# Kernel optimization log

Measured on AMD Instinct MI355X. Metric: run time of the kernel, lower is better.

## Reference

```python
import jax, jax.numpy as jnp
import numpy as np

H = 128
R = 14
B = 2048
TYPES = ['operator', 'table', 'column', 'predicate', 'operation', 'literal', 'numeral']
SIZES = {'operator': 100000, 'table': 20000, 'column': 120000, 'predicate': 60000,
         'operation': 100000, 'literal': 50000, 'numeral': 50000}
FEAT = {'operator': 4, 'table': 2, 'column': 10, 'predicate': 4, 'operation': 8,
        'literal': 1, 'numeral': 1}
# (name, src_type, dst_type, num_edges), order matches edge_type_mapping in the torch module
EDGES = [('ei_scannedby', 'table', 'operator', 100000),
         ('ei_pred_filters', 'predicate', 'operator', 100000),
         ('ei_outputby', 'column', 'operator', 100000),
         ('ei_col_connects', 'column', 'operation', 100000),
         ('ei_calledby', 'operator', 'operator', 100000),
         ('ei_op_filters', 'operation', 'operator', 100000),
         ('ei_op_connects', 'operation', 'predicate', 100000),
         ('ei_lit_connects', 'literal', 'operation', 100000),
         ('ei_num_connects', 'numeral', 'operation', 100000),
         ('ei_lit_self', 'literal', 'literal', 50000),
         ('ei_num_self', 'numeral', 'numeral', 50000),
         ('ei_tab_self', 'table', 'table', 20000),
         ('ei_col_self', 'column', 'column', 120000),
         ('ei_pred_self', 'predicate', 'predicate', 60000)]
OFFS = {}
_o = 0
for _t in TYPES:
    OFFS[_t] = _o
    _o += SIZES[_t]
N_TOTAL = _o


def setup_inputs():
    key = jax.random.key(0)
    ks = iter(jax.random.split(key, 64))
    inp = {}
    for t in TYPES:
        inp['x_' + t] = jax.random.normal(next(ks), (SIZES[t], FEAT[t]), jnp.float32)
    for name, s, d, E in EDGES:
        src = jax.random.randint(next(ks), (E,), 0, SIZES[s], jnp.int32)
        dst = jax.random.randint(next(ks), (E,), 0, SIZES[d], jnp.int32)
        inp[name] = jnp.stack([src, dst])
    inp['batch_operator'] = jnp.sort(
        jax.random.randint(next(ks), (SIZES['operator'],), 0, B, jnp.int32))

    def lin_w(k, din, dout):
        s = 1.0 / float(np.sqrt(din))
        return jax.random.uniform(k, (din, dout), jnp.float32, -s, s)

    for t in TYPES:
        inp['W_' + t] = lin_w(next(ks), FEAT[t], H)
        inp['b_' + t] = jnp.zeros((H,), jnp.float32)
    for c in ('c1', 'c2'):
        inp[c + '_root'] = lin_w(next(ks), H, H)
        inp[c + '_rel'] = jax.random.normal(next(ks), (R, H, H), jnp.float32) / float(np.sqrt(H))
        inp[c + '_bias'] = jnp.zeros((H,), jnp.float32)
    inp['n1_g'] = jnp.ones((H,), jnp.float32); inp['n1_b'] = jnp.zeros((H,), jnp.float32)
    inp['n2_g'] = jnp.ones((H,), jnp.float32); inp['n2_b'] = jnp.zeros((H,), jnp.float32)
    inp['W_lin'] = lin_w(next(ks), H, 1)
    inp['b_lin'] = jnp.zeros((1,), jnp.float32)
    return inp


def layer_norm(x, g, b, eps=1e-5):
    mu = jnp.mean(x, axis=-1, keepdims=True)
    var = jnp.var(x, axis=-1, keepdims=True)
    return (x - mu) * jax.lax.rsqrt(var + eps) * g + b


def rgcn(x, rel_edges, w_root, w_rel, bias):
    # PyG RGCNConv: root transform + per-relation gather -> GEMM -> scatter-mean into dst
    out = x @ w_root
    for r, (src, dst) in enumerate(rel_edges):
        msg = x[src] @ w_rel[r]  # [E_r, H]
        agg = jax.ops.segment_sum(msg, dst, num_segments=N_TOTAL)
        cnt = jax.ops.segment_sum(jnp.ones(src.shape, x.dtype), dst, num_segments=N_TOTAL)
        out = out + agg / jnp.maximum(cnt, 1.0)[:, None]
    return out + bias


def reference(x_operator, x_table, x_column, x_predicate, x_operation, x_literal, x_numeral,
              ei_scannedby, ei_pred_filters, ei_outputby, ei_col_connects, ei_calledby,
              ei_op_filters, ei_op_connects, ei_lit_connects, ei_num_connects, ei_lit_self,
              ei_num_self, ei_tab_self, ei_col_self, ei_pred_self, batch_operator,
              W_operator, b_operator, W_table, b_table, W_column, b_column,
              W_predicate, b_predicate, W_operation, b_operation, W_literal, b_literal,
              W_numeral, b_numeral, c1_root, c1_rel, c1_bias, c2_root, c2_rel, c2_bias,
              n1_g, n1_b, n2_g, n2_b, W_lin, b_lin):
    # per-node-type input embedding, then concat in fixed type order
    x = jnp.concatenate([
        x_operator @ W_operator + b_operator,
        x_table @ W_table + b_table,
        x_column @ W_column + b_column,
        x_predicate @ W_predicate + b_predicate,
        x_operation @ W_operation + b_operation,
        x_literal @ W_literal + b_literal,
        x_numeral @ W_numeral + b_numeral], axis=0)
    eis = [ei_scannedby, ei_pred_filters, ei_outputby, ei_col_connects, ei_calledby,
           ei_op_filters, ei_op_connects, ei_lit_connects, ei_num_connects, ei_lit_self,
           ei_num_self, ei_tab_self, ei_col_self, ei_pred_self]
    rel_edges = [(e[0] + OFFS[s], e[1] + OFFS[d]) for e, (_, s, d, _) in zip(eis, EDGES)]
    h = rgcn(x, rel_edges, c1_root, c1_rel, c1_bias)
    h = layer_norm(jax.nn.elu(h), n1_g, n1_b)  # dropout is identity in eval mode
    h = rgcn(h, rel_edges, c2_root, c2_rel, c2_bias)
    h = layer_norm(jax.nn.elu(h), n2_g, n2_b)
    op = h[:SIZES['operator']]  # operator offset is 0
    cnt = jax.ops.segment_sum(jnp.ones((op.shape[0],), op.dtype), batch_operator, num_segments=B)
    pooled = jax.ops.segment_sum(op, batch_operator, num_segments=B) / jnp.maximum(cnt, 1.0)[:, None]
    return (pooled @ W_lin + b_lin)[:, 0]  # [B]
```

## Files before the change

### kernel.cpp

```cpp
#include <hip/hip_runtime.h>
#include <hip/hip_bf16.h>
#include <math.h>

#define HD 128
#define N_OP 100000
#define N_L1 400000
#define NB 2048
#define CNT_TOT 1160000
#define EDG_TOT 1100000

typedef short short8 __attribute__((ext_vector_type(8)));
typedef float floatx4 __attribute__((ext_vector_type(4)));

static const int REL_E[14]    = {100000,100000,100000,100000,100000,100000,100000,100000,100000,50000,50000,20000,120000,60000};
static const int REL_DSZ[14]  = {100000,100000,100000,100000,100000,100000,60000,100000,100000,50000,50000,20000,120000,60000};
static const int CNT_OFF[14]  = {0,100000,200000,300000,400000,500000,600000,660000,760000,860000,910000,960000,980000,1100000};
static const int SRC_T[14] = {1,3,2,2,0,4,4,5,6,5,6,1,2,3};
static const int TF[7]  = {4,2,10,4,8,1,1};
static const size_t AGR_OFF[14] = {0,200000,600000,1600000,2600000,3000000,3800000,4280000,4380000,0,0,4480000,4520000,5720000};
#define AGR_TOT 5960000
static const int RELW[14] = {4,7,12,93,23,28,70,104,106,-1,-1,40,54,79};
static const int RELI[14] = {6,11,22,103,27,36,78,105,107,-1,-1,42,64,83};
static const int ROOTW[5] = {0,38,44,66,85};
static const int ROOTB[5] = {37,43,65,84,108};
#define WL1_ROWS 109

__device__ inline unsigned short f2bf(float f) {
  union { float f; unsigned int u; } v; v.f = f;
  unsigned int r = v.u + 0x7FFF + ((v.u >> 16) & 1);
  return (unsigned short)(r >> 16);
}
__device__ inline float bfu2f(unsigned short u) {
  union { unsigned int i; float f; } v; v.i = ((unsigned int)u) << 16; return v.f;
}

struct CJob { const int* dst; int coff; int E; int blk0; };
struct CombJob { const float* A; const float* bin; const float* Mtx; const float* extra; float* Wout; float* bout; int F; };
struct PrepPack {
  CJob j[12];
  int bblk0;
  int wstart;
  const int* batch; float* pcnt; int nop;
  CombJob c[17];
};

__global__ void prep_k(PrepPack P, const float* __restrict__ c2root,
                       const float* __restrict__ c2rel, __hip_bfloat16* __restrict__ Wt,
                       int* __restrict__ ICNT) {
  int b = blockIdx.x;
  if (b >= P.wstart) {
    int wj = b - P.wstart;
    if (wj < 17) {
      if (threadIdx.x >= 128) return;
      CombJob J = P.c[wj];
      int c = threadIdx.x;
      for (int f = 0; f <= J.F; ++f) {
        const float* arow = (f < J.F) ? &J.A[f * HD] : J.bin;
        float s = (f < J.F) ? 0.f : (J.extra ? J.extra[c] : 0.f);
        for (int k = 0; k < HD; ++k) s = fmaf(arow[k], J.Mtx[k * HD + c], s);
        if (f < J.F) J.Wout[f * HD + c] = s;
        else J.bout[c] = s;
      }
    } else {
      const int RID[6] = {-1, 0, 1, 2, 4, 5};
      int j = wj - 17;
      const float* W = (j == 0) ? c2root : (c2rel + (size_t)RID[j] * HD * HD);
      __hip_bfloat16* o = Wt + (size_t)j * 16384;
      for (int i = threadIdx.x; i < 16384; i += 256) {
        int i8 = i & 7;
        int ln = (i >> 3) & 63;
        int k4 = (i >> 9) & 3;
        int nt = i >> 11;
        int ln15 = ln & 15, quad = ln >> 4;
        int k = k4 * 32 + quad * 8 + i8;
        int n = nt * 16 + ln15;
        o[i] = __float2bfloat16(W[k * 128 + n]);
      }
    }
    return;
  }
  if (b >= P.bblk0) {
    int i = (b - P.bblk0) * 256 + threadIdx.x;
    if (i < P.nop) atomicAdd(&P.pcnt[P.batch[i]], 1.0f);
    return;
  }
  int ji = 0;
#pragma unroll
  for (int i = 1; i < 12; ++i) if (b >= P.j[i].blk0) ji = i;
  CJob J = P.j[ji];
  int e = (b - J.blk0) * 256 + threadIdx.x;
  if (e < J.E) atomicAdd(&ICNT[J.coff + J.dst[e]], 1);
}

#define SCAN_BLK 1024
__global__ void scan1(const int* __restrict__ in, int* __restrict__ out,
                      int* __restrict__ bsum, int n) {
  __shared__ int sh[256];
  int t = threadIdx.x;
  int base = blockIdx.x * SCAN_BLK + t * 4;
  int v0 = 0, v1 = 0, v2 = 0, v3 = 0;
  if (base + 3 < n) { int4 q = *(const int4*)&in[base]; v0 = q.x; v1 = q.y; v2 = q.z; v3 = q.w; }
  else {
    if (base < n) v0 = in[base];
    if (base + 1 < n) v1 = in[base + 1];
    if (base + 2 < n) v2 = in[base + 2];
    if (base + 3 < n) v3 = in[base + 3];
  }
  int ts = v0 + v1 + v2 + v3;
  sh[t] = ts; __syncthreads();
  for (int o = 1; o < 256; o <<= 1) {
    int x = (t >= o) ? sh[t - o] : 0;
    __syncthreads();
    sh[t] += x;
    __syncthreads();
  }
  int excl = sh[t] - ts;
  if (base < n) out[base] = excl;
  if (base + 1 < n) out[base + 1] = excl + v0;
  if (base + 2 < n) out[base + 2] = excl + v0 + v1;
  if (base + 3 < n) out[base + 3] = excl + v0 + v1 + v2;
  if (t == 255) bsum[blockIdx.x] = sh[255];
}

__global__ void scan3b(int* __restrict__ CUR, int2* __restrict__ OFF2,
                       const int* __restrict__ ICNT, const int* __restrict__ bs, int n) {
  __shared__ int sh[4];
  const int j = blockIdx.x, t = threadIdx.x;
  int s = 0;
  for (int i = t; i < j; i += 256) s += bs[i];
#pragma unroll
  for (int m = 32; m >= 1; m >>= 1) s += __shfl_xor(s, m, 64);
  if ((t & 63) == 0) sh[t >> 6] = s;
  __syncthreads();
  int base = sh[0] + sh[1] + sh[2] + sh[3];
  int i0 = j * SCAN_BLK + t * 4;
#pragma unroll
  for (int k = 0; k < 4; ++k) {
    int i = i0 + k;
    if (i < n) {
      int o = CUR[i] + base;
      CUR[i] = o;
      OFF2[i] = make_int2(o, ICNT[i]);
    }
  }
}

struct FJob { const int* src; const int* dst; int coff; int E; int blk0; };
struct FPackK { FJob j[12]; };

__global__ void fill_k(FPackK P, int* __restrict__ CUR, int* __restrict__ EDG) {
  int b = blockIdx.x;
  int ji = 0;
#pragma unroll
  for (int i = 1; i < 12; ++i) if (b >= P.j[i].blk0) ji = i;
  FJob J = P.j[ji];
  int e = (b - J.blk0) * 256 + threadIdx.x;
  if (e < J.E) {
    int pos = atomicAdd(&CUR[J.coff + J.dst[e]], 1);
    EDG[pos] = J.src[e];
  }
}

struct GJob { const float* x; float* agr; int coff; int D; int F; int blk0; };
struct GPack { GJob j[12]; };

template <int F>
__device__ inline void gathF(const float* __restrict__ x, float* __restrict__ agr,
                             const int* __restrict__ EDG, int2 oc, int d) {
  if (oc.y == 0) return;
  float s[F];
#pragma unroll
  for (int f = 0; f < F; ++f) s[f] = 0.f;
  for (int e = 0; e < oc.y; ++e) {
    int si = EDG[oc.x + e];
    const float* xp = &x[(size_t)si * F];
#pragma unroll
    for (int f = 0; f < F; ++f) s[f] += xp[f];
  }
  float rc = 1.0f / (float)oc.y;
  float* ap = &agr[(size_t)d * F];
#pragma unroll
  for (int f = 0; f < F; ++f) ap[f] = s[f] * rc;
}

__global__ void gather_all(GPack P, const int2* __restrict__ OFF2, const int* __restrict__ EDG) {
  int b = blockIdx.x;
  int ji = 0;
#pragma unroll
  for (int i = 1; i < 12; ++i) if (b >= P.j[i].blk0) ji = i;
  GJob J = P.j[ji];
  int d = (b - J.blk0) * 256 + threadIdx.x;
  if (d >= J.D) return;
  int2 oc = OFF2[J.coff + d];
  switch (J.F) {
    case 1:  gathF<1>(J.x, J.agr, EDG, oc, d); break;
    case 2:  gathF<2>(J.x, J.agr, EDG, oc, d); break;
    case 4:  gathF<4>(J.x, J.agr, EDG, oc, d); break;
    case 8:  gathF<8>(J.x, J.agr, EDG, oc, d); break;
    default: gathF<10>(J.x, J.agr, EDG, oc, d); break;
  }
}

struct L1v2 {
  const float* x0; const float* x1; const float* x2; const float* x3; const float* x4;
  const float* AGR; const float* WL1; const int2* OFF2;
  const float* g; const float* b;
  unsigned short* Hb;
};

__device__ inline void ldv2(float* s, const float* __restrict__ p) {
  float2 v = *(const float2*)p; s[0] = v.x; s[1] = v.y;
}
__device__ inline void ldv4(float* s, const float* __restrict__ p) {
  float4 v = *(const float4*)p; s[0] = v.x; s[1] = v.y; s[2] = v.z; s[3] = v.w;
}
__device__ inline void relF1(float* s, const float* __restrict__ agr,
                             const int2* __restrict__ OFF2, int cb, int row) {
  if (OFF2[cb + row].y > 0) { s[0] = agr[row]; s[1] = 1.f; }
  else { s[0] = 0.f; s[1] = 0.f; }
}
__device__ inline void relF2(float* s, const float* __restrict__ agr,
                             const int2* __restrict__ OFF2, int cb, int row) {
  if (OFF2[cb + row].y > 0) { ldv2(s, &agr[(size_t)row * 2]); s[2] = 1.f; }
  else { s[0] = s[1] = s[2] = 0.f; }
}
__device__ inline void relF4(float* s, const float* __restrict__ agr,
                             const int2* __restrict__ OFF2, int cb, int row) {
  if (OFF2[cb + row].y > 0) { ldv4(s, &agr[(size_t)row * 4]); s[4] = 1.f; }
  else {
#pragma unroll
    for (int f = 0; f < 5; ++f) s[f] = 0.f;
  }
}
__device__ inline void relF8(float* s, const float* __restrict__ agr,
                             const int2* __restrict__ OFF2, int cb, int row) {
  if (OFF2[cb + row].y > 0) {
    ldv4(s, &agr[(size_t)row * 8]); ldv4(s + 4, &agr[(size_t)row * 8 + 4]); s[8] = 1.f;
  } else {
#pragma unroll
    for (int f = 0; f < 9; ++f) s[f] = 0.f;
  }
}
__device__ inline void relF10(float* s, const float* __restrict__ agr,
                              const int2* __restrict__ OFF2, int cb, int row) {
  if (OFF2[cb + row].y > 0) {
    const float* p = &agr[(size_t)row * 10];
#pragma unroll
    for (int j = 0; j < 5; ++j) ldv2(s + 2 * j, p + 2 * j);
    s[10] = 1.f;
  } else {
#pragma unroll
    for (int f = 0; f < 11; ++f) s[f] = 0.f;
  }
}

template <int KT>
__device__ inline void l1_dot8(const float* __restrict__ Ls, const float (&s)[KT],
                               int c4, float (&a)[8]) {
  {
    float4 w0 = *(const float4*)&Ls[KT * 128 + c4];
    float4 w1 = *(const float4*)&Ls[KT * 128 + c4 + 64];
    a[0] = w0.x; a[1] = w0.y; a[2] = w0.z; a[3] = w0.w;
    a[4] = w1.x; a[5] = w1.y; a[6] = w1.z; a[7] = w1.w;
  }
#pragma unroll
  for (int k = 0; k < KT; ++k) {
    float4 w0 = *(const float4*)&Ls[k * 128 + c4];
    float4 w1 = *(const float4*)&Ls[k * 128 + c4 + 64];
    a[0] = fmaf(s[k], w0.x, a[0]); a[1] = fmaf(s[k], w0.y, a[1]);
    a[2] = fmaf(s[k], w0.z, a[2]); a[3] = fmaf(s[k], w0.w, a[3]);
    a[4] = fmaf(s[k], w1.x, a[4]); a[5] = fmaf(s[k], w1.y, a[5]);
    a[6] = fmaf(s[k], w1.z, a[6]); a[7] = fmaf(s[k], w1.w, a[7]);
  }
}

__device__ inline void l1_fin8(float (&a)[8], int c4, const float* __restrict__ g,
                               const float* __restrict__ bb,
                               unsigned short* __restrict__ Hb, int orow) {
  float p = 0.f, q = 0.f;
#pragma unroll
  for (int j = 0; j < 8; ++j) {
    a[j] = (a[j] > 0.f) ? a[j] : (expf(a[j]) - 1.f);
    p += a[j]; q += a[j] * a[j];
  }
#pragma unroll
  for (int m = 8; m >= 1; m >>= 1) {
    p += __shfl_xor(p, m, 64);
    q += __shfl_xor(q, m, 64);
  }
  float mean = p * (1.0f / HD);
  float var = q * (1.0f / HD) - mean * mean;
  float rstd = rsqrtf(var + 1e-5f);
  float4 g0 = *(const float4*)&g[c4], g1 = *(const float4*)&g[c4 + 64];
  float4 b0 = *(const float4*)&bb[c4], b1 = *(const float4*)&bb[c4 + 64];
  float gg[8] = {g0.x, g0.y, g0.z, g0.w, g1.x, g1.y, g1.z, g1.w};
  float bv[8] = {b0.x, b0.y, b0.z, b0.w, b1.x, b1.y, b1.z, b1.w};
  float o[8];
#pragma unroll
  for (int j = 0; j < 8; ++j) o[j] = (a[j] - mean) * rstd * gg[j] + bv[j];
  uint2 lo, hi;
  lo.x = (unsigned int)f2bf(o[0]) | ((unsigned int)f2bf(o[1]) << 16);
  lo.y = (unsigned int)f2bf(o[2]) | ((unsigned int)f2bf(o[3]) << 16);
  hi.x = (unsigned int)f2bf(o[4]) | ((unsigned int)f2bf(o[5]) << 16);
  hi.y = (unsigned int)f2bf(o[6]) | ((unsigned int)f2bf(o[7]) << 16);
  *(uint2*)&Hb[(size_t)orow * HD + c4] = lo;
  *(uint2*)&Hb[(size_t)orow * HD + c4 + 64] = hi;
}

__global__ __launch_bounds__(256) void layer1_v5(L1v2 A) {
  __shared__ float Ls[38 * 128];
  const int b = blockIdx.x, t = threadIdx.x;
  const int wv = t >> 6, ln = t & 63;
  const int sub = ln >> 4, c4 = (ln & 15) * 4;
  int type, seg;
  if (b < 1563) { type = 0; seg = b; }
  else if (b < 1876) { type = 1; seg = b - 1563; }
  else if (b < 3751) { type = 2; seg = b - 1876; }
  else if (b < 4689) { type = 3; seg = b - 3751; }
  else { type = 4; seg = b - 4689; }
  const int NR[5] = {38, 6, 22, 19, 24};
  const int RB[5] = {0, 38, 44, 66, 85};
  const int TR[5] = {100000, 20000, 120000, 60000, 100000};
  const int OB[5] = {0, 100000, 120000, 240000, 300000};
  {
    const float4* src = (const float4*)(A.WL1 + RB[type] * 128);
    float4* dst = (float4*)Ls;
    int n4 = NR[type] * 32;
    for (int i = t; i < n4; i += 256) dst[i] = src[i];
  }
  __syncthreads();
  const int row0 = seg * 64, M = TR[type], ob = OB[type];

  if (type == 0) {
#pragma unroll
    for (int it = 0; it < 4; ++it) {
      int row = row0 + it * 16 + wv * 4 + sub;
      if (row >= M) continue;
      float s[37];
      ldv4(s, &A.x0[(size_t)row * 4]);
      relF2(s + 4, A.AGR + 0, A.OFF2, 0, row);
      relF4(s + 7, A.AGR + 200000, A.OFF2, 100000, row);
      relF10(s + 12, A.AGR + 600000, A.OFF2, 200000, row);
      relF4(s + 23, A.AGR + 2600000, A.OFF2, 400000, row);
      relF8(s + 28, A.AGR + 3000000, A.OFF2, 500000, row);
      float a[8];
      l1_dot8<37>(Ls, s, c4, a);
      l1_fin8(a, c4, A.g, A.b, A.Hb, ob + row);
    }
  } else if (type == 1) {
#pragma unroll
    for (int it = 0; it < 4; ++it) {
      int row = row0 + it * 16 + wv * 4 + sub;
      if (row >= M) continue;
      float s[5];
      ldv2(s, &A.x1[(size_t)row * 2]);
      relF2(s + 2, A.AGR + 4480000, A.OFF2, 960000, row);
      float a[8];
      l1_dot8<5>(Ls, s, c4, a);
      l1_fin8(a, c4, A.g, A.b, A.Hb, ob + row);
    }
  } else if (type == 2) {
#pragma unroll
    for (int it = 0; it < 4; ++it) {
      int row = row0 + it * 16 + wv * 4 + sub;
      if (row >= M) continue;
      float s[21];
      const float* p = &A.x2[(size_t)row * 10];
#pragma unroll
      for (int j = 0; j < 5; ++j) ldv2(s + 2 * j, p + 2 * j);
      relF10(s + 10, A.AGR + 4520000, A.OFF2, 980000, row);
      float a[8];
      l1_dot8<21>(Ls, s, c4, a);
      l1_fin8(a, c4, A.g, A.b, A.Hb, ob + row);
    }
  } else if (type == 3) {
#pragma unroll
    for (int it = 0; it < 4; ++it) {
      int row = row0 + it * 16 + wv * 4 + sub;
      if (row >= M) continue;
      float s[18];
      ldv4(s, &A.x3[(size_t)row * 4]);
      relF8(s + 4, A.AGR + 3800000, A.OFF2, 600000, row);
      relF4(s + 13, A.AGR + 5720000, A.OFF2, 1100000, row);
      float a[8];
      l1_dot8<18>(Ls, s, c4, a);
      l1_fin8(a, c4, A.g, A.b, A.Hb, ob + row);
    }
  } else {
#pragma unroll
    for (int it = 0; it < 4; ++it) {
      int row = row0 + it * 16 + wv * 4 + sub;
      if (row >= M) continue;
      float s[23];
      ldv4(s, &A.x4[(size_t)row * 8]);
      ldv4(s + 4, &A.x4[(size_t)row * 8 + 4]);
      relF10(s + 8, A.AGR + 1600000, A.OFF2, 300000, row);
      relF1(s + 19, A.AGR + 4280000, A.OFF2, 660000, row);
      relF1(s + 21, A.AGR + 4380000, A.OFF2, 760000, row);
      float a[8];
      l1_dot8<23>(Ls, s, c4, a);
      l1_fin8(a, c4, A.g, A.b, A.Hb, ob + row);
    }
  }
}

__global__ __launch_bounds__(256, 4)
void l2_fused(const unsigned short* __restrict__ Hb, const unsigned short* __restrict__ Wt,
              const int2* __restrict__ OFF2, const int* __restrict__ EDG,
              const float* __restrict__ c2bias, const float* __restrict__ n2g,
              const float* __restrict__ n2b, const float* __restrict__ Wl,
              const int* __restrict__ batch, float* __restrict__ accb, int M) {
  const int CSR_OFF[5] = {0, 100000, 200000, 400000, 500000};
  const int SOFF[5]    = {100000, 240000, 120000, 0, 300000};
  const int t = threadIdx.x, wv = t >> 6, ln = t & 63;
  const int quad = ln >> 4, ln15 = ln & 15, q8 = quad * 8;
  const int m0 = blockIdx.x * 64;
  const int rowA = m0 + wv * 16 + ln15;

  int2 ocs[5];
#pragma unroll
  for (int r = 0; r < 5; ++r)
    ocs[r] = (rowA < M) ? OFF2[CSR_OFF[r] + rowA] : make_int2(0, 0);

  float bias_c[8], gw[8];
  float pg = 0.f, pb = 0.f;
#pragma unroll
  for (int nt = 0; nt < 8; ++nt) {
    int col = nt * 16 + ln15;
    float wl = Wl[col], gc = n2g[col], bc = n2b[col];
    bias_c[nt] = c2bias[col];
    gw[nt] = gc * wl;
    pg += gc * wl;
    pb += bc * wl;
  }
#pragma unroll
  for (int m = 8; m >= 1; m >>= 1) {
    pg += __shfl_xor(pg, m, 64);
    pb += __shfl_xor(pb, m, 64);
  }

  floatx4 acc[8];
#pragma unroll
  for (int b = 0; b < 8; ++b) acc[b] = (floatx4){0.f, 0.f, 0.f, 0.f};

  for (int term = 0; term < 6; ++term) {
    short8 afr[4];
    if (term == 0) {
      if (rowA < M) {
#pragma unroll
        for (int k4 = 0; k4 < 4; ++k4)
          afr[k4] = *(const short8*)&Hb[(size_t)rowA * HD + k4 * 32 + q8];
      } else {
#pragma unroll
        for (int k4 = 0; k4 < 4; ++k4)
#pragma unroll
          for (int j = 0; j < 8; ++j) afr[k4][j] = 0;
      }
    } else {
      float sum[4][8];
#pragma unroll
      for (int k4 = 0; k4 < 4; ++k4)
#pragma unroll
        for (int j = 0; j < 8; ++j) sum[k4][j] = 0.f;
      int2 oc = ocs[term - 1];
      if (oc.y > 0) {
        int so = SOFF[term - 1];
        for (int e = 0; e < oc.y; ++e) {
          size_t s = (size_t)(EDG[oc.x + e] + so);
#pragma unroll
          for (int k4 = 0; k4 < 4; ++k4) {
            short8 h = *(const short8*)&Hb[s * HD + k4 * 32 + q8];
#pragma unroll
            for (int j = 0; j < 8; ++j) sum[k4][j] += bfu2f((unsigned short)h[j]);
          }
        }
        float rc = 1.0f / (float)oc.y;
#pragma unroll
        for (int k4 = 0; k4 < 4; ++k4)
#pragma unroll
          for (int j = 0; j < 8; ++j) sum[k4][j] *= rc;
      }
#pragma unroll
      for (int k4 = 0; k4 < 4; ++k4)
#pragma unroll
        for (int j = 0; j < 8; ++j) afr[k4][j] = (short)f2bf(sum[k4][j]);
    }

    const unsigned short* wb = Wt + (size_t)term * 16384 + (size_t)ln * 8;
#pragma unroll
    for (int nt = 0; nt < 8; ++nt) {
      short8 b0 = *(const short8*)(wb + nt * 2048 + 0 * 512);
      short8 b1 = *(const short8*)(wb + nt * 2048 + 1 * 512);
      short8 b2 = *(const short8*)(wb + nt * 2048 + 2 * 512);
      short8 b3 = *(const short8*)(wb + nt * 2048 + 3 * 512);
      acc[nt] = __builtin_amdgcn_mfma_f32_16x16x32_bf16(afr[0], b0, acc[nt], 0, 0, 0);
      acc[nt] = __builtin_amdgcn_mfma_f32_16x16x32_bf16(afr[1], b1, acc[nt], 0, 0, 0);
      acc[nt] = __builtin_amdgcn_mfma_f32_16x16x32_bf16(afr[2], b2, acc[nt], 0, 0, 0);
      acc[nt] = __builtin_amdgcn_mfma_f32_16x16x32_bf16(afr[3], b3, acc[nt], 0, 0, 0);
    }
  }

#pragma unroll
  for (int r = 0; r < 4; ++r) {
    int rowD = m0 + wv * 16 + quad * 4 + r;
    float p = 0.f, q = 0.f, s1 = 0.f;
#pragma unroll
    for (int nt = 0; nt < 8; ++nt) {
      float v = acc[nt][r] + bias_c[nt];
      float e = (v > 0.f) ? v : (expf(v) - 1.f);
      p += e; q += e * e; s1 += e * gw[nt];
    }
#pragma unroll
    for (int m = 8; m >= 1; m >>= 1) {
      p += __shfl_xor(p, m, 64);
      q += __shfl_xor(q, m, 64);
      s1 += __shfl_xor(s1, m, 64);
    }
    if (ln15 == 0 && rowD < M) {
      float mean = p * (1.0f / HD);
      float var = q * (1.0f / HD) - mean * mean;
      float rstd = rsqrtf(var + 1e-5f);
      float o = rstd * (s1 - mean * pg) + pb;
      atomicAdd(&accb[batch[rowD]], o);
    }
  }
}

__global__ void final_kernel(const float* __restrict__ accb, const float* __restrict__ pcnt,
                             const float* __restrict__ bl, float* __restrict__ out) {
  int b = blockIdx.x * 256 + threadIdx.x;
  if (b < NB) out[b] = accb[b] / fmaxf(pcnt[b], 1.0f) + bl[0];
}

extern "C" void kernel_launch(void* const* d_in, const int* in_sizes, int n_in,
                              void* d_out, int out_size, void* d_ws, size_t ws_size,
                              hipStream_t stream) {
  const float* xt[7];
  for (int t = 0; t < 7; ++t) xt[t] = (const float*)d_in[t];
  const int* ei[14];
  for (int r = 0; r < 14; ++r) ei[r] = (const int*)d_in[7 + r];
  const int* batch = (const int*)d_in[21];
  const float* Wemb[7]; const float* bemb[7];
  for (int t = 0; t < 7; ++t) { Wemb[t] = (const float*)d_in[22 + 2 * t]; bemb[t] = (const float*)d_in[23 + 2 * t]; }
  const float* c_root[2] = {(const float*)d_in[36], (const float*)d_in[39]};
  const float* c_rel[2]  = {(const float*)d_in[37], (const float*)d_in[40]};
  const float* c_bias[2] = {(const float*)d_in[38], (const float*)d_in[41]};
  const float* ng[2] = {(const float*)d_in[42], (const float*)d_in[44]};
  const float* nbv[2] = {(const float*)d_in[43], (const float*)d_in[45]};
  const float* Wlin = (const float*)d_in[46];
  const float* blin = (const float*)d_in[47];
  float* out = (float*)d_out;

  char* base = (char*)d_ws;
  size_t off = 0;
  auto alloc = [&](size_t bytes) -> void* {
    void* p = base + off;
    off += (bytes + 255) & ~(size_t)255;
    return p;
  };
  __hip_bfloat16* Hb = (__hip_bfloat16*)alloc((size_t)N_L1 * HD * 2);
  float* AGR  = (float*)alloc((size_t)AGR_TOT * 4);
  int*   ICNT = (int*)alloc((size_t)CNT_TOT * 4 + (size_t)2 * NB * 4);
  float* ACC  = (float*)(ICNT + CNT_TOT);
  float* PCNT = ACC + NB;
  int*   CUR  = (int*)alloc((size_t)CNT_TOT * 4);
  int2*  OFF2 = (int2*)alloc((size_t)CNT_TOT * 8);
  int*   EDG  = (int*)alloc((size_t)EDG_TOT * 4);
  int*   BS   = (int*)alloc((size_t)1152 * 4);
  float* WL1  = (float*)alloc((size_t)WL1_ROWS * 128 * 4);
  __hip_bfloat16* WT3 = (__hip_bfloat16*)alloc((size_t)6 * 16384 * 2);

  static const int l1_rels[12] = {0,1,2,3,4,5,6,7,8,11,12,13};

  hipMemsetAsync(ICNT, 0, (size_t)CNT_TOT * 4 + (size_t)2 * NB * 4, stream);

  PrepPack PP;
  int blk = 0;
  for (int q = 0; q < 12; ++q) {
    int r = l1_rels[q];
    PP.j[q].dst = ei[r] + REL_E[r];
    PP.j[q].coff = CNT_OFF[r];
    PP.j[q].E = REL_E[r];
    PP.j[q].blk0 = blk;
    blk += (REL_E[r] + 255) / 256;
  }
  PP.bblk0 = blk; PP.batch = batch; PP.pcnt = PCNT; PP.nop = N_OP;
  blk += (N_OP + 255) / 256;
  PP.wstart = blk;
  for (int q = 0; q < 12; ++q) {
    int r = l1_rels[q]; int t = SRC_T[r];
    CombJob& J = PP.c[q];
    J.A = Wemb[t]; J.bin = bemb[t]; J.Mtx = c_rel[0] + (size_t)r * HD * HD;
    J.extra = nullptr;
    J.Wout = WL1 + (size_t)RELW[r] * 128;
    J.bout = WL1 + (size_t)RELI[r] * 128;
    J.F = TF[t];
  }
  for (int t = 0; t < 5; ++t) {
    CombJob& J = PP.c[12 + t];
    J.A = Wemb[t]; J.bin = bemb[t]; J.Mtx = c_root[0];
    J.extra = c_bias[0];
    J.Wout = WL1 + (size_t)ROOTW[t] * 128;
    J.bout = WL1 + (size_t)ROOTB[t] * 128;
    J.F = TF[t];
  }
  prep_k<<<blk + 23, 256, 0, stream>>>(PP, c_root[1], c_rel[1], WT3, ICNT);

  int nb1 = (CNT_TOT + SCAN_BLK - 1) / SCAN_BLK;
  scan1<<<nb1, 256, 0, stream>>>(ICNT, CUR, BS, CNT_TOT);
  scan3b<<<nb1, 256, 0, stream>>>(CUR, OFF2, ICNT, BS, CNT_TOT);

  FPackK FP;
  blk = 0;
  for (int q = 0; q < 12; ++q) {
    int r = l1_rels[q];
    FP.j[q].src = ei[r];
    FP.j[q].dst = ei[r] + REL_E[r];
    FP.j[q].coff = CNT_OFF[r];
    FP.j[q].E = REL_E[r];
    FP.j[q].blk0 = blk;
    blk += (REL_E[r] + 255) / 256;
  }
  fill_k<<<blk, 256, 0, stream>>>(FP, CUR, EDG);

  GPack GP;
  blk = 0;
  for (int q = 0; q < 12; ++q) {
    int r = l1_rels[q]; int t = SRC_T[r];
    GP.j[q].x = xt[t];
    GP.j[q].agr = AGR + AGR_OFF[r];
    GP.j[q].coff = CNT_OFF[r];
    GP.j[q].D = REL_DSZ[r];
    GP.j[q].F = TF[t];
    GP.j[q].blk0 = blk;
    blk += (REL_DSZ[r] + 255) / 256;
  }
  gather_all<<<blk, 256, 0, stream>>>(GP, OFF2, EDG);

  L1v2 A;
  A.x0 = xt[0]; A.x1 = xt[1]; A.x2 = xt[2]; A.x3 = xt[3]; A.x4 = xt[4];
  A.AGR = AGR; A.WL1 = WL1; A.OFF2 = OFF2;
  A.g = ng[0]; A.b = nbv[0]; A.Hb = (unsigned short*)Hb;
  layer1_v5<<<6252, 256, 0, stream>>>(A);

  l2_fused<<<(N_OP + 63) / 64, 256, 0, stream>>>(
      (const unsigned short*)Hb, (const unsigned short*)WT3,
      OFF2, EDG, c_bias[1], ng[1], nbv[1], Wlin, batch, ACC, N_OP);

  final_kernel<<<(NB + 255) / 256, 256, 0, stream>>>(ACC, PCNT, blin, out);
}
```

Measured before the change: 602.9 us.

## Prefetch first neighbor row per relation and vectorize feature gathers

In the layer-2 fused kernel, the first source index of each relation is loaded up front and the first neighbor row of the next term is fetched during the current term's MFMAs, so gather latency overlaps compute. For single-edge rows the prefetched bf16 row is used directly, skipping the float round trip. The layer-1 gather also switches to float2/float4 vector loads and stores. This adds register pressure under launch_bounds(256,4), and the float2/float4 casts assume rows are aligned to the vector width.

```diff
diff --git a/kernel.cpp b/kernel.cpp
--- a/kernel.cpp
+++ b/kernel.cpp
@@ -174,13 +174,40 @@
   for (int e = 0; e < oc.y; ++e) {
     int si = EDG[oc.x + e];
     const float* xp = &x[(size_t)si * F];
-#pragma unroll
-    for (int f = 0; f < F; ++f) s[f] += xp[f];
+    if (F == 1) {
+      s[0] += xp[0];
+    } else if (F == 2) {
+      float2 v = *(const float2*)xp; s[0] += v.x; s[1] += v.y;
+    } else if (F == 4) {
+      float4 v = *(const float4*)xp;
+      s[0] += v.x; s[1] += v.y; s[2] += v.z; s[3] += v.w;
+    } else if (F == 8) {
+      float4 v0 = *(const float4*)xp, v1 = *(const float4*)(xp + 4);
+      s[0] += v0.x; s[1] += v0.y; s[2] += v0.z; s[3] += v0.w;
+      s[4] += v1.x; s[5] += v1.y; s[6] += v1.z; s[7] += v1.w;
+    } else {
+#pragma unroll
+      for (int j = 0; j < F / 2; ++j) {
+        float2 v = *(const float2*)(xp + 2 * j);
+        s[2 * j] += v.x; s[2 * j + 1] += v.y;
+      }
+    }
   }
   float rc = 1.0f / (float)oc.y;
+#pragma unroll
+  for (int f = 0; f < F; ++f) s[f] *= rc;
   float* ap = &agr[(size_t)d * F];
-#pragma unroll
-  for (int f = 0; f < F; ++f) ap[f] = s[f] * rc;
+  if (F == 1) { ap[0] = s[0]; }
+  else if (F == 2) { *(float2*)ap = make_float2(s[0], s[1]); }
+  else if (F == 4) { *(float4*)ap = make_float4(s[0], s[1], s[2], s[3]); }
+  else if (F == 8) {
+    *(float4*)ap = make_float4(s[0], s[1], s[2], s[3]);
+    *(float4*)(ap + 4) = make_float4(s[4], s[5], s[6], s[7]);
+  } else {
+#pragma unroll
+    for (int j = 0; j < F / 2; ++j)
+      *(float2*)(ap + 2 * j) = make_float2(s[2 * j], s[2 * j + 1]);
+  }
 }
 
 __global__ void gather_all(GPack P, const int2* __restrict__ OFF2, const int* __restrict__ EDG) {
@@ -421,6 +448,10 @@
 #pragma unroll
   for (int r = 0; r < 5; ++r)
     ocs[r] = (rowA < M) ? OFF2[CSR_OFF[r] + rowA] : make_int2(0, 0);
+  int pre[5];
+#pragma unroll
+  for (int r = 0; r < 5; ++r)
+    pre[r] = (ocs[r].y > 0) ? EDG[ocs[r].x] : 0;
 
   float bias_c[8], gw[8];
   float pg = 0.f, pb = 0.f;
@@ -443,29 +474,49 @@
 #pragma unroll
   for (int b = 0; b < 8; ++b) acc[b] = (floatx4){0.f, 0.f, 0.f, 0.f};
 
+  short8 nbuf[4];
+  if (rowA < M) {
+#pragma unroll
+    for (int k4 = 0; k4 < 4; ++k4)
+      nbuf[k4] = *(const short8*)&Hb[(size_t)rowA * HD + k4 * 32 + q8];
+  } else {
+#pragma unroll
+    for (int k4 = 0; k4 < 4; ++k4)
+#pragma unroll
+      for (int j = 0; j < 8; ++j) nbuf[k4][j] = 0;
+  }
+
+#pragma unroll
   for (int term = 0; term < 6; ++term) {
     short8 afr[4];
-    if (term == 0) {
-      if (rowA < M) {
+#pragma unroll
+    for (int k4 = 0; k4 < 4; ++k4) afr[k4] = nbuf[k4];
+
+    if (term < 5) {
+      int2 ocn = ocs[term];
+      if (ocn.y > 0) {
+        size_t s = (size_t)(pre[term] + SOFF[term]);
 #pragma unroll
         for (int k4 = 0; k4 < 4; ++k4)
-          afr[k4] = *(const short8*)&Hb[(size_t)rowA * HD + k4 * 32 + q8];
+          nbuf[k4] = *(const short8*)&Hb[s * HD + k4 * 32 + q8];
       } else {
 #pragma unroll
         for (int k4 = 0; k4 < 4; ++k4)
 #pragma unroll
-          for (int j = 0; j < 8; ++j) afr[k4][j] = 0;
+          for (int j = 0; j < 8; ++j) nbuf[k4][j] = 0;
       }
-    } else {
-      float sum[4][8];
-#pragma unroll
-      for (int k4 = 0; k4 < 4; ++k4)
-#pragma unroll
-        for (int j = 0; j < 8; ++j) sum[k4][j] = 0.f;
+    }
+
+    if (term > 0) {
       int2 oc = ocs[term - 1];
-      if (oc.y > 0) {
+      if (oc.y > 1) {
+        float sum[4][8];
+#pragma unroll
+        for (int k4 = 0; k4 < 4; ++k4)
+#pragma unroll
+          for (int j = 0; j < 8; ++j) sum[k4][j] = bfu2f((unsigned short)afr[k4][j]);
         int so = SOFF[term - 1];
-        for (int e = 0; e < oc.y; ++e) {
+        for (int e = 1; e < oc.y; ++e) {
           size_t s = (size_t)(EDG[oc.x + e] + so);
 #pragma unroll
           for (int k4 = 0; k4 < 4; ++k4) {
@@ -478,12 +529,8 @@
 #pragma unroll
         for (int k4 = 0; k4 < 4; ++k4)
 #pragma unroll
-          for (int j = 0; j < 8; ++j) sum[k4][j] *= rc;
+          for (int j = 0; j < 8; ++j) afr[k4][j] = (short)f2bf(sum[k4][j] * rc);
       }
-#pragma unroll
-      for (int k4 = 0; k4 < 4; ++k4)
-#pragma unroll
-        for (int j = 0; j < 8; ++j) afr[k4][j] = (short)f2bf(sum[k4][j]);
     }
 
     const unsigned short* wb = Wt + (size_t)term * 16384 + (size_t)ln * 8;
```

Result: no change. 600.4 us (-0.4%).
